# Performance work log

Measured on AMD Instinct MI355X. Metric: run time of the kernel, lower is better.

## Reference

```python
import jax, jax.numpy as jnp
import numpy as np

EMBED_DIM = 1024


def setup_inputs() -> dict:
    key = jax.random.key(0)
    ks = jax.random.split(key, 9)
    d = EMBED_DIM
    s = 1.0 / np.sqrt(d)
    x = jax.random.normal(ks[0], (4, 2048, d), dtype=jnp.float32)
    # nn.Linear weights are [out, in]; we store them transposed for x @ W
    Wq = jax.random.uniform(ks[1], (d, d), jnp.float32, -s, s)
    bq = jax.random.uniform(ks[2], (d,), jnp.float32, -s, s)
    Wk = jax.random.uniform(ks[3], (d, d), jnp.float32, -s, s)
    bk = jax.random.uniform(ks[4], (d,), jnp.float32, -s, s)
    Wv = jax.random.uniform(ks[5], (d, d), jnp.float32, -s, s)
    bv = jax.random.uniform(ks[6], (d,), jnp.float32, -s, s)
    Wo = jax.random.uniform(ks[7], (d, d), jnp.float32, -s, s)
    bo = jax.random.uniform(ks[8], (d,), jnp.float32, -s, s)
    return {"x": x, "Wq": Wq, "bq": bq, "Wk": Wk, "bk": bk,
            "Wv": Wv, "bv": bv, "Wo": Wo, "bo": bo}


def reference(x, Wq, bq, Wk, bk, Wv, bv, Wo, bo):
    b, seq_len, d = x.shape
    scaling = 1.0 / jnp.sqrt(jnp.float32(d))
    q = x @ Wq + bq  # [b, s, d]
    k = x @ Wk + bk
    v = x @ Wv + bv
    scores = jnp.einsum('bqd,bkd->bqk', q, k) * scaling  # [b, s, s]
    causal = jnp.tril(jnp.ones((seq_len, seq_len), dtype=bool))
    scores = jnp.where(causal, scores, -jnp.inf)
    attn = jax.nn.softmax(scores, axis=-1)
    out = jnp.einsum('bqk,bkd->bqd', attn, v)
    return out @ Wo + bo
```

## Files before the change

kernel.cpp:

```cpp
#include <hip/hip_runtime.h>
#include <stdint.h>

typedef __bf16 bf16_t;
typedef __bf16 bf16x8 __attribute__((ext_vector_type(8)));
typedef __bf16 bf16x4 __attribute__((ext_vector_type(4)));
typedef float  f32x4  __attribute__((ext_vector_type(4)));

#define DEV __device__ __forceinline__

constexpr int S = 2048, D = 1024, BATCH = 4, MF = BATCH * S;

DEV void gload16(const void* g, void* l) {
  __builtin_amdgcn_global_load_lds(
      (const __attribute__((address_space(1))) void*)g,
      (__attribute__((address_space(3))) void*)(uint32_t)(uintptr_t)l,
      16, 0, 0);
}

template<int EP, int NSUB>
DEV void gemm_body(int tm, int tn, int bz,
                   const bf16_t* __restrict__ A, const bf16_t* __restrict__ B,
                   void* __restrict__ C0, void* __restrict__ C1,
                   void* __restrict__ C2, const float* __restrict__ aux,
                   int K, int kmax, bf16_t* ldsA, bf16_t* ldsB)
{
  const int m0 = tm * 128, n0 = tn * 128;
  const int tid  = threadIdx.x;
  const int lane = tid & 63;
  const int wave = tid >> 6;
  const int wm = wave & 1, wn = wave >> 1;
  const int l8r = lane >> 3;
  const int swz = ((lane & 7) ^ (lane >> 3)) * 8;
  const int cl  = lane & 15;
  const int qd  = lane >> 4;
  const int ch0 = ((qd ^ (cl & 7)) * 8);

  f32x4 acc[4][4] = {};

  for (int k0 = 0; k0 < kmax; k0 += 64 * NSUB) {
    #pragma unroll
    for (int h = 0; h < NSUB; ++h) {
      #pragma unroll
      for (int t = 0; t < 4; ++t) {
        const int rb = wave * 4 + t;
        gload16(A + (long)(m0 + rb * 8 + l8r) * K + (k0 + h * 64 + swz),
                &ldsA[h * 8192 + rb * 512]);
        gload16(B + (long)(n0 + rb * 8 + l8r) * K + (k0 + h * 64 + swz),
                &ldsB[h * 8192 + rb * 512]);
      }
    }
    __syncthreads();
    #pragma unroll
    for (int h = 0; h < NSUB; ++h) {
      #pragma unroll
      for (int kk = 0; kk < 64; kk += 32) {
        bf16x8 af[4], bg[4];
        #pragma unroll
        for (int i = 0; i < 4; ++i)
          af[i] = *(const bf16x8*)&ldsA[h * 8192 + (wm * 64 + i * 16 + cl) * 64 + (ch0 ^ kk)];
        #pragma unroll
        for (int j = 0; j < 4; ++j)
          bg[j] = *(const bf16x8*)&ldsB[h * 8192 + (wn * 64 + j * 16 + cl) * 64 + (ch0 ^ kk)];
        #pragma unroll
        for (int i = 0; i < 4; ++i)
          #pragma unroll
          for (int j = 0; j < 4; ++j)
            acc[i][j] = __builtin_amdgcn_mfma_f32_16x16x32_bf16(af[i], bg[j], acc[i][j], 0, 0, 0);
      }
    }
    __syncthreads();
  }

  #pragma unroll
  for (int i = 0; i < 4; ++i) {
    const int gm0 = m0 + wm * 64 + i * 16 + qd * 4;

    if (EP == 1) {
      uint8_t* q8 = (uint8_t*)C0;
      uint8_t* k8 = (uint8_t*)C1;
      bf16_t* vwT = (bf16_t*)C2;
      #pragma unroll
      for (int j = 0; j < 4; ++j) {
        const int gn  = n0 + wn * 64 + j * 16 + cl;
        const int sec = gn >> 10, ln = gn & 1023;
        const float bn = aux[gn];
        if (sec == 2) {
          const int z = gm0 >> 11, s0 = gm0 & 2047;
          bf16x4 v4;
          #pragma unroll
          for (int r = 0; r < 4; ++r) v4[r] = (bf16_t)(acc[i][j][r] + bn);
          *(bf16x4*)&vwT[((long)z * D + ln) * S + s0] = v4;
        } else {
          uint8_t* dst = (sec == 0) ? q8 : k8;
          #pragma unroll
          for (int r = 0; r < 4; ++r) {
            const float v = acc[i][j][r] + bn;
            const int p = __builtin_amdgcn_cvt_pk_fp8_f32(v, v, 0, false);
            dst[(long)(gm0 + r) * D + ln] = (uint8_t)(p & 0xFF);
          }
        }
      }
    }

    if (EP == 5) {
      float* out = (float*)C0 + (long)bz * S * D;
      const float* bo = (const float*)C1;
      const float* invl_l = aux;
      float scl[4];
      #pragma unroll
      for (int r = 0; r < 4; ++r) scl[r] = invl_l[wm * 64 + i * 16 + qd * 4 + r];
      #pragma unroll
      for (int j = 0; j < 4; ++j) {
        const int gn = n0 + wn * 64 + j * 16 + cl;
        const float bn = bo[gn];
        #pragma unroll
        for (int r = 0; r < 4; ++r)
          out[(long)(gm0 + r) * D + gn] = acc[i][j][r] * scl[r] + bn;
      }
    }

    if (EP == 4) {
      bf16_t* Co = (bf16_t*)C0;
      #pragma unroll
      for (int j = 0; j < 4; ++j) {
        const int gn = n0 + wn * 64 + j * 16 + cl;
        #pragma unroll
        for (int r = 0; r < 4; ++r)
          Co[(long)(gm0 + r) * D + gn] = (bf16_t)acc[i][j][r];
      }
    }
  }
}

__global__ __launch_bounds__(256, 4) void gemm_qkv(
    const bf16_t* __restrict__ A, const bf16_t* __restrict__ B,
    uint8_t* q8, uint8_t* k8, bf16_t* vwT, const float* __restrict__ bias)
{
  __shared__ __align__(16) bf16_t lA[128 * 64], lB[128 * 64];
  gemm_body<1, 1>(blockIdx.x, blockIdx.y, 0, A, B, q8, k8, vwT, bias,
                  1024, 1024, lA, lB);
}

__global__ __launch_bounds__(256, 4) void gemm_sc8(
    const uint8_t* __restrict__ q8g, const uint8_t* __restrict__ k8g,
    bf16_t* __restrict__ probs_g, float* __restrict__ part)
{
  __shared__ __align__(16) uint8_t lA[2][128 * 64], lB[2][128 * 64];
  const int l = blockIdx.x, xcd = l & 7, idx = l >> 3;
  const int bz = xcd >> 1;
  const int t  = (xcd & 1) * 68 + idx;
  int tm = (int)((sqrtf(8.0f * t + 1.0f) - 1.0f) * 0.5f);
  while ((tm + 1) * (tm + 2) / 2 <= t) ++tm;
  while (tm * (tm + 1) / 2 > t) --tm;
  const int tn = t - tm * (tm + 1) / 2;
  const int m0 = tm * 128, n0 = tn * 128;
  const uint8_t* q8 = q8g + (long)bz * S * D;
  const uint8_t* k8 = k8g + (long)bz * S * D;

  const int tid  = threadIdx.x;
  const int lane = tid & 63;
  const int wave = tid >> 6;
  const int wm = wave & 1, wn = wave >> 1;
  const int srow = lane >> 2;
  const int sgr  = (lane & 3) ^ ((lane >> 3) & 3);
  const int cl = lane & 15, qd = lane >> 4;
  const int sfr = (cl >> 1) & 3;
  const int half8 = (qd & 1) * 8;

  f32x4 acc[4][4] = {};

  for (int k0 = 0; k0 < 1024; k0 += 128) {
    #pragma unroll
    for (int h = 0; h < 2; ++h) {
      #pragma unroll
      for (int tt = 0; tt < 2; ++tt) {
        const int rb = wave * 2 + tt;
        const int gr = rb * 16 + srow;
        gload16(q8 + (long)(m0 + gr) * 1024 + k0 + h * 64 + sgr * 16,
                &lA[h][rb * 1024]);
        gload16(k8 + (long)(n0 + gr) * 1024 + k0 + h * 64 + sgr * 16,
                &lB[h][rb * 1024]);
      }
    }
    __syncthreads();
    #pragma unroll
    for (int h = 0; h < 2; ++h) {
      #pragma unroll
      for (int kk = 0; kk < 2; ++kk) {
        long a[4], b[4];
        const int pg = ((kk << 1) + (qd >> 1)) ^ sfr;
        #pragma unroll
        for (int i = 0; i < 4; ++i)
          a[i] = *(const long*)&lA[h][(wm * 64 + i * 16 + cl) * 64 + pg * 16 + half8];
        #pragma unroll
        for (int j = 0; j < 4; ++j)
          b[j] = *(const long*)&lB[h][(wn * 64 + j * 16 + cl) * 64 + pg * 16 + half8];
        #pragma unroll
        for (int i = 0; i < 4; ++i)
          #pragma unroll
          for (int j = 0; j < 4; ++j)
            acc[i][j] = __builtin_amdgcn_mfma_f32_16x16x32_fp8_fp8(a[i], b[j], acc[i][j], 0, 0, 0);
      }
    }
    __syncthreads();
  }

  bf16_t* probs = probs_g + (long)bz * S * S;
  #pragma unroll
  for (int i = 0; i < 4; ++i) {
    const int gm0 = m0 + wm * 64 + i * 16 + qd * 4;
    float ls[4] = {0.f, 0.f, 0.f, 0.f};
    #pragma unroll
    for (int j = 0; j < 4; ++j) {
      const int gn = n0 + wn * 64 + j * 16 + cl;
      #pragma unroll
      for (int r = 0; r < 4; ++r) {
        const int gm = gm0 + r;
        const float e = (gn <= gm) ? __expf(acc[i][j][r] * 0.03125f) : 0.0f;
        probs[(long)gm * S + gn] = (bf16_t)e;
        ls[r] += e;
      }
    }
    #pragma unroll
    for (int r = 0; r < 4; ++r) {
      float v = ls[r];
      v += __shfl_xor(v, 1); v += __shfl_xor(v, 2);
      v += __shfl_xor(v, 4); v += __shfl_xor(v, 8);
      if (cl == 0)
        part[((long)bz * S + (gm0 + r)) * 32 + tn * 2 + wn] = v;
    }
  }
}

__global__ __launch_bounds__(256, 2) void gemm_pv_out(
    const bf16_t* __restrict__ probs, const bf16_t* __restrict__ vwT,
    float* out, const float* __restrict__ part, const float* __restrict__ bo)
{
  __shared__ __align__(16) bf16_t lA[2 * 128 * 64], lB[2 * 128 * 64];
  __shared__ float invl_s[128];
  const int l = blockIdx.x, xcd = l & 7, idx = l >> 3;
  const int bz = xcd >> 1, half = xcd & 1;
  const int g = (idx >> 3) & 3, tn = idx & 7;
  const int tm = (idx < 32) ? (15 - half - 2 * g) : (2 * g + half);
  const int kmax = (tm + 1) * 128;

  if (threadIdx.x < 128) {
    const int row = tm * 128 + threadIdx.x;
    const int cnt = (tm + 1) * 2;
    const float* p = part + ((long)bz * S + row) * 32;
    float s = 0.f;
    for (int j = 0; j < cnt; ++j) s += p[j];
    invl_s[threadIdx.x] = 1.0f / s;
  }
  __syncthreads();

  gemm_body<5, 2>(tm, tn, bz, probs + (long)bz * S * S, vwT + (long)bz * D * S,
                  out, (void*)bo, nullptr, invl_s, 2048, kmax, lA, lB);
}

__global__ __launch_bounds__(256, 4) void gemm_wvo(
    const bf16_t* __restrict__ WoT, const bf16_t* __restrict__ WvN,
    bf16_t* WvoT)
{
  __shared__ __align__(16) bf16_t lA[128 * 64], lB[128 * 64];
  gemm_body<4, 1>(blockIdx.x, blockIdx.y, 0, WoT, WvN, WvoT, nullptr, nullptr,
                  nullptr, 1024, 1024, lA, lB);
}

__global__ __launch_bounds__(256) void cvt_x(
    const float4* __restrict__ in, bf16x4* __restrict__ out, int n4)
{
  const int i = blockIdx.x * 256 + threadIdx.x;
  if (i >= n4) return;
  float4 f = in[i];
  bf16x4 o;
  o.x = (__bf16)f.x; o.y = (__bf16)f.y; o.z = (__bf16)f.z; o.w = (__bf16)f.w;
  out[i] = o;
}

__global__ __launch_bounds__(256) void cvt_w_t4(
    const float* __restrict__ W0, const float* __restrict__ W1,
    const float* __restrict__ W2, const float* __restrict__ W3,
    bf16_t* __restrict__ dst)
{
  const int zmap[4] = {0, 1, 3, 4};
  const float* W = (blockIdx.z == 0) ? W0 : (blockIdx.z == 1) ? W1
                 : (blockIdx.z == 2) ? W2 : W3;
  bf16_t* WT = dst + (size_t)zmap[blockIdx.z] * D * D;
  const int bx = blockIdx.x, by = blockIdx.y;
  const int tx = threadIdx.x & 31, ty = threadIdx.x >> 5;

  if (blockIdx.z == 2) {
    #pragma unroll
    for (int dy = 0; dy < 32; dy += 8) {
      const long idx = (long)(by * 32 + ty + dy) * 1024 + bx * 32 + tx;
      WT[idx] = (bf16_t)W[idx];
    }
    return;
  }

  __shared__ float t[32][33];
  #pragma unroll
  for (int dy = 0; dy < 32; dy += 8)
    t[ty + dy][tx] = W[(long)(by * 32 + ty + dy) * 1024 + bx * 32 + tx];
  __syncthreads();
  #pragma unroll
  for (int dy = 0; dy < 32; dy += 8)
    WT[(long)(bx * 32 + ty + dy) * 1024 + by * 32 + tx] = (bf16_t)t[tx][ty + dy];
}

__global__ __launch_bounds__(256) void bias_build(
    const float* __restrict__ bq, const float* __restrict__ bk,
    const float* __restrict__ bv, const bf16_t* __restrict__ WoT,
    float* __restrict__ o)
{
  const int b = blockIdx.x;
  if (b >= 256) {
    const int i = (b - 256) * 256 + threadIdx.x;
    o[i] = bq[i];
    o[1024 + i] = bk[i];
    return;
  }
  const int wave = threadIdx.x >> 6, lane = threadIdx.x & 63;
  const int c = b * 4 + wave;
  const bf16_t* row = WoT + (long)c * 1024 + lane * 16;
  const float*  bvp = bv + lane * 16;
  float s = 0.f;
  #pragma unroll
  for (int j = 0; j < 16; ++j) s += bvp[j] * (float)row[j];
  #pragma unroll
  for (int sh = 32; sh > 0; sh >>= 1) s += __shfl_xor(s, sh, 64);
  if (lane == 0) o[2048 + c] = s;
}

extern "C" void kernel_launch(void* const* d_in, const int* in_sizes, int n_in,
                              void* d_out, int out_size, void* d_ws, size_t ws_size,
                              hipStream_t stream) {
  const float* x  = (const float*)d_in[0];
  const float* Wq = (const float*)d_in[1];
  const float* bq = (const float*)d_in[2];
  const float* Wk = (const float*)d_in[3];
  const float* bk = (const float*)d_in[4];
  const float* Wv = (const float*)d_in[5];
  const float* bv = (const float*)d_in[6];
  const float* Wo = (const float*)d_in[7];
  const float* bo = (const float*)d_in[8];
  float* out = (float*)d_out;

  size_t off = 0;
  auto alloc = [&](size_t bytes) -> void* {
    void* p = (char*)d_ws + off;
    off += (bytes + 255) & ~(size_t)255;
    return p;
  };
  bf16_t* x_b   = (bf16_t*)alloc((size_t)MF * D * 2);
  bf16_t* Wall  = (bf16_t*)alloc((size_t)5 * D * D * 2);
  float*  bqkv  = (float*) alloc((size_t)3 * D * 4);
  uint8_t* q8   = (uint8_t*)alloc((size_t)MF * D);
  uint8_t* k8   = (uint8_t*)alloc((size_t)MF * D);
  bf16_t* vwT_b = (bf16_t*)alloc((size_t)BATCH * D * S * 2);
  bf16_t* probs = (bf16_t*)alloc((size_t)BATCH * S * S * 2);
  float*  part  = (float*) alloc((size_t)MF * 32 * 4);
  bf16_t* WqkvT = Wall;
  bf16_t* WvoT  = Wall + (size_t)2 * D * D;
  bf16_t* WvN   = Wall + (size_t)3 * D * D;
  bf16_t* WoT   = Wall + (size_t)4 * D * D;

  cvt_x<<<dim3((MF * D / 4 + 255) / 256), 256, 0, stream>>>(
      (const float4*)x, (bf16x4*)x_b, MF * D / 4);
  cvt_w_t4<<<dim3(32, 32, 4), 256, 0, stream>>>(Wq, Wk, Wv, Wo, Wall);
  bias_build<<<dim3(260), 256, 0, stream>>>(bq, bk, bv, WoT, bqkv);

  gemm_wvo<<<dim3(8, 8), 256, 0, stream>>>(WoT, WvN, WvoT);

  gemm_qkv<<<dim3(64, 24), 256, 0, stream>>>(x_b, WqkvT, q8, k8, vwT_b, bqkv);

  gemm_sc8<<<dim3(544), 256, 0, stream>>>(q8, k8, probs, part);

  gemm_pv_out<<<dim3(512), 256, 0, stream>>>(probs, vwT_b, out, part, bo);
}
```

Before: 243.5 us.

## Merge preamble kernels into one launch and double score-GEMM K-tile depth

Three setup kernels (x conversion, weight transpose/convert, bias build) are fused into a single preamble launch, and the bias build now reads Wo directly instead of the transposed copy, which removes its dependency on the transpose finishing first. Separately, the fp8 score GEMM stages 256 K-columns per sync instead of 128, halving barriers but doubling LDS and lowering the occupancy bound from 4 to 2 blocks. The strided Wo reads in the bias path are uncoalesced, and the lower occupancy may reduce latency hiding.

New measurement: 261.4 us. 1.07x slower.

```diff
diff --git a/kernel.cpp b/kernel.cpp
--- a/kernel.cpp
+++ b/kernel.cpp
@@ -141,11 +141,11 @@
                   1024, 1024, lA, lB);
 }
 
-__global__ __launch_bounds__(256, 4) void gemm_sc8(
+__global__ __launch_bounds__(256, 2) void gemm_sc8(
     const uint8_t* __restrict__ q8g, const uint8_t* __restrict__ k8g,
     bf16_t* __restrict__ probs_g, float* __restrict__ part)
 {
-  __shared__ __align__(16) uint8_t lA[2][128 * 64], lB[2][128 * 64];
+  __shared__ __align__(16) uint8_t lA[4][128 * 64], lB[4][128 * 64];
   const int l = blockIdx.x, xcd = l & 7, idx = l >> 3;
   const int bz = xcd >> 1;
   const int t  = (xcd & 1) * 68 + idx;
@@ -169,9 +169,9 @@
 
   f32x4 acc[4][4] = {};
 
-  for (int k0 = 0; k0 < 1024; k0 += 128) {
-    #pragma unroll
-    for (int h = 0; h < 2; ++h) {
+  for (int k0 = 0; k0 < 1024; k0 += 256) {
+    #pragma unroll
+    for (int h = 0; h < 4; ++h) {
       #pragma unroll
       for (int tt = 0; tt < 2; ++tt) {
         const int rb = wave * 2 + tt;
@@ -184,7 +184,7 @@
     }
     __syncthreads();
     #pragma unroll
-    for (int h = 0; h < 2; ++h) {
+    for (int h = 0; h < 4; ++h) {
       #pragma unroll
       for (int kk = 0; kk < 2; ++kk) {
         long a[4], b[4];
@@ -267,67 +267,68 @@
                   nullptr, 1024, 1024, lA, lB);
 }
 
-__global__ __launch_bounds__(256) void cvt_x(
-    const float4* __restrict__ in, bf16x4* __restrict__ out, int n4)
-{
-  const int i = blockIdx.x * 256 + threadIdx.x;
-  if (i >= n4) return;
-  float4 f = in[i];
-  bf16x4 o;
-  o.x = (__bf16)f.x; o.y = (__bf16)f.y; o.z = (__bf16)f.z; o.w = (__bf16)f.w;
-  out[i] = o;
-}
-
-__global__ __launch_bounds__(256) void cvt_w_t4(
-    const float* __restrict__ W0, const float* __restrict__ W1,
-    const float* __restrict__ W2, const float* __restrict__ W3,
-    bf16_t* __restrict__ dst)
-{
-  const int zmap[4] = {0, 1, 3, 4};
-  const float* W = (blockIdx.z == 0) ? W0 : (blockIdx.z == 1) ? W1
-                 : (blockIdx.z == 2) ? W2 : W3;
-  bf16_t* WT = dst + (size_t)zmap[blockIdx.z] * D * D;
-  const int bx = blockIdx.x, by = blockIdx.y;
-  const int tx = threadIdx.x & 31, ty = threadIdx.x >> 5;
-
-  if (blockIdx.z == 2) {
-    #pragma unroll
-    for (int dy = 0; dy < 32; dy += 8) {
-      const long idx = (long)(by * 32 + ty + dy) * 1024 + bx * 32 + tx;
-      WT[idx] = (bf16_t)W[idx];
-    }
+__global__ __launch_bounds__(256) void preamble(
+    const float* __restrict__ x, bf16x4* __restrict__ x_b,
+    const float* __restrict__ Wq, const float* __restrict__ Wk,
+    const float* __restrict__ Wv, const float* __restrict__ Wo,
+    bf16_t* __restrict__ Wall,
+    const float* __restrict__ bq, const float* __restrict__ bk,
+    const float* __restrict__ bv, float* __restrict__ o)
+{
+  __shared__ float t[32][33];
+  const int b = blockIdx.x;
+  const int tid = threadIdx.x;
+
+  if (b < 8192) {
+    const int i = b * 256 + tid;
+    float4 f = ((const float4*)x)[i];
+    bf16x4 v;
+    v.x = (__bf16)f.x; v.y = (__bf16)f.y; v.z = (__bf16)f.z; v.w = (__bf16)f.w;
+    x_b[i] = v;
     return;
   }
 
-  __shared__ float t[32][33];
-  #pragma unroll
-  for (int dy = 0; dy < 32; dy += 8)
-    t[ty + dy][tx] = W[(long)(by * 32 + ty + dy) * 1024 + bx * 32 + tx];
-  __syncthreads();
-  #pragma unroll
-  for (int dy = 0; dy < 32; dy += 8)
-    WT[(long)(bx * 32 + ty + dy) * 1024 + by * 32 + tx] = (bf16_t)t[tx][ty + dy];
-}
-
-__global__ __launch_bounds__(256) void bias_build(
-    const float* __restrict__ bq, const float* __restrict__ bk,
-    const float* __restrict__ bv, const bf16_t* __restrict__ WoT,
-    float* __restrict__ o)
-{
-  const int b = blockIdx.x;
-  if (b >= 256) {
-    const int i = (b - 256) * 256 + threadIdx.x;
+  if (b < 12288) {
+    const int idx = b - 8192;
+    const int bx = idx & 31, by = (idx >> 5) & 31, z = idx >> 10;
+    const int zmap[4] = {0, 1, 3, 4};
+    const float* W = (z == 0) ? Wq : (z == 1) ? Wk : (z == 2) ? Wv : Wo;
+    bf16_t* WT = Wall + (size_t)zmap[z] * D * D;
+    const int tx = tid & 31, ty = tid >> 5;
+
+    if (z == 2) {
+      #pragma unroll
+      for (int dy = 0; dy < 32; dy += 8) {
+        const long i2 = (long)(by * 32 + ty + dy) * 1024 + bx * 32 + tx;
+        WT[i2] = (bf16_t)W[i2];
+      }
+      return;
+    }
+    #pragma unroll
+    for (int dy = 0; dy < 32; dy += 8)
+      t[ty + dy][tx] = W[(long)(by * 32 + ty + dy) * 1024 + bx * 32 + tx];
+    __syncthreads();
+    #pragma unroll
+    for (int dy = 0; dy < 32; dy += 8)
+      WT[(long)(bx * 32 + ty + dy) * 1024 + by * 32 + tx] = (bf16_t)t[tx][ty + dy];
+    return;
+  }
+
+  const int bb = b - 12288;
+  if (bb >= 256) {
+    const int i = (bb - 256) * 256 + tid;
     o[i] = bq[i];
     o[1024 + i] = bk[i];
     return;
   }
-  const int wave = threadIdx.x >> 6, lane = threadIdx.x & 63;
-  const int c = b * 4 + wave;
-  const bf16_t* row = WoT + (long)c * 1024 + lane * 16;
-  const float*  bvp = bv + lane * 16;
+  const int wave = tid >> 6, lane = tid & 63;
+  const int c = bb * 4 + wave;
   float s = 0.f;
   #pragma unroll
-  for (int j = 0; j < 16; ++j) s += bvp[j] * (float)row[j];
+  for (int j = 0; j < 16; ++j) {
+    const int e = lane * 16 + j;
+    s += bv[e] * (float)(bf16_t)Wo[(long)e * 1024 + c];
+  }
   #pragma unroll
   for (int sh = 32; sh > 0; sh >>= 1) s += __shfl_xor(s, sh, 64);
   if (lane == 0) o[2048 + c] = s;
@@ -366,10 +367,8 @@
   bf16_t* WvN   = Wall + (size_t)3 * D * D;
   bf16_t* WoT   = Wall + (size_t)4 * D * D;
 
-  cvt_x<<<dim3((MF * D / 4 + 255) / 256), 256, 0, stream>>>(
-      (const float4*)x, (bf16x4*)x_b, MF * D / 4);
-  cvt_w_t4<<<dim3(32, 32, 4), 256, 0, stream>>>(Wq, Wk, Wv, Wo, Wall);
-  bias_build<<<dim3(260), 256, 0, stream>>>(bq, bk, bv, WoT, bqkv);
+  preamble<<<dim3(12548), 256, 0, stream>>>(
+      x, (bf16x4*)x_b, Wq, Wk, Wv, Wo, Wall, bq, bk, bv, bqkv);
 
   gemm_wvo<<<dim3(8, 8), 256, 0, stream>>>(WoT, WvN, WvoT);
 
```
